# Performance work log

Measured on AMD Instinct MI355X. Metric: run time of the kernel, lower is better.

## Reference

```python
import jax, jax.numpy as jnp
import numpy as np

D = 768          # embed_dim
NH = 12          # num_heads
HD = D // NH     # head_dim = 64
DEPTH = 12
PATCH = 16
IMG = 256
NP_ = (IMG // PATCH) ** 2   # 256 spatial patches
PTOT = NP_ + 1              # 257 tokens per frame (cls + patches)
SCALE = HD ** -0.5
EPS = 1e-5


def _attn(xb, w, b):
    # xb: (B, S, D); w: (D, 3D); b: (3D,)
    B, S, _ = xb.shape
    qkv = (xb @ w + b).reshape(B, S, 3, NH, HD).transpose(2, 0, 3, 1, 4)
    q, k, v = qkv[0], qkv[1], qkv[2]             # each (B, NH, S, HD)
    a = jax.nn.softmax(jnp.einsum('bhqd,bhkd->bhqk', q, k) * SCALE, axis=-1)
    o = jnp.einsum('bhqk,bhkd->bhqd', a, v)      # (B, NH, S, HD)
    return o.transpose(0, 2, 1, 3).reshape(B, S, D)


def setup_inputs() -> dict:
    key = jax.random.key(0)
    ks = jax.random.split(key, 16)
    std = 0.02
    inp = {
        'x': jax.random.normal(ks[0], (2, 16, 3, IMG, IMG), jnp.float32),
        'patch_w': jax.random.normal(ks[1], (D, 3, PATCH, PATCH), jnp.float32) * std,
        'patch_b': jnp.zeros((D,), jnp.float32),
        'cls_token': jax.random.normal(ks[2], (1, 1, D), jnp.float32) * std,
        'pos_embed': jax.random.normal(ks[3], (1, PTOT, D), jnp.float32) * std,
        'time_embed': jax.random.normal(ks[4], (1, 16, D), jnp.float32) * std,
        'wqkv_s': jax.random.normal(ks[5], (DEPTH, D, 3 * D), jnp.float32) * std,
        'bqkv_s': jnp.zeros((DEPTH, 3 * D), jnp.float32),
        'wqkv_t': jax.random.normal(ks[6], (DEPTH, D, 3 * D), jnp.float32) * std,
        'bqkv_t': jnp.zeros((DEPTH, 3 * D), jnp.float32),
        'wproj': jax.random.normal(ks[7], (DEPTH, D, D), jnp.float32) * std,
        'bproj': jnp.zeros((DEPTH, D), jnp.float32),
        'ln_g': jnp.ones((D,), jnp.float32),
        'ln_b': jnp.zeros((D,), jnp.float32),
        'head_w': jax.random.normal(ks[8], (1, D), jnp.float32) * std,
        'head_b': jnp.zeros((1,), jnp.float32),
    }
    return inp


def reference(x, patch_w, patch_b, cls_token, pos_embed, time_embed,
              wqkv_s, bqkv_s, wqkv_t, bqkv_t, wproj, bproj,
              ln_g, ln_b, head_w, head_b):
    N, T, C, H, W = x.shape
    Hp = H // PATCH
    # patch embed: 16x16 stride-16 conv as unfold + matmul
    xp = x.reshape(N * T, C, Hp, PATCH, Hp, PATCH)
    xp = xp.transpose(0, 2, 4, 1, 3, 5).reshape(N * T, NP_, C * PATCH * PATCH)
    tok = xp @ patch_w.reshape(D, -1).T + patch_b          # (N*T, 256, D)
    tok = tok.reshape(N, T, NP_, D)
    cls = jnp.broadcast_to(cls_token, (N, T, 1, D))
    h = jnp.concatenate([cls, tok], axis=2)                # (N, T, 257, D)
    h = h + pos_embed[:, None]                             # (1,1,257,D) broadcast
    h = h + time_embed[:, :T][:, :, None]                  # (1,T,1,D) broadcast
    h = h.reshape(N, T * PTOT, D)

    for i in range(DEPTH):
        x4 = h.reshape(N, T, PTOT, D)
        # spatial attention within each frame
        xs = x4.reshape(N * T, PTOT, D)
        so = _attn(xs, wqkv_s[i], bqkv_s[i]) @ wproj[i] + bproj[i]
        x4 = x4 + so.reshape(N, T, PTOT, D)
        # temporal attention across frames per spatial location
        xt = x4.transpose(0, 2, 1, 3).reshape(N * PTOT, T, D)
        to = _attn(xt, wqkv_t[i], bqkv_t[i]) @ wproj[i] + bproj[i]
        x4 = x4 + to.reshape(N, PTOT, T, D).transpose(0, 2, 1, 3)
        h = x4.reshape(N, T * PTOT, D)

    mu = h.mean(axis=-1, keepdims=True)
    var = ((h - mu) ** 2).mean(axis=-1, keepdims=True)
    h = (h - mu) * jax.lax.rsqrt(var + EPS) * ln_g + ln_b
    cls_tok = h.reshape(N, T, PTOT, D)[:, :, 0, :].mean(axis=1)   # (N, D)
    logits = cls_tok @ head_w.T + head_b                          # (N, 1)
    return logits
```

## Files before the change

kernel.cpp:

```cpp
#include <hip/hip_runtime.h>
#include <hip/hip_bf16.h>
#include <math.h>

namespace {

constexpr int D    = 768;
constexpr int NH   = 12;
constexpr int PTOT = 257;
constexpr int NB   = 2;
constexpr int TT   = 16;
constexpr int NTOK = NB * TT * PTOT;
constexpr int NPAT = NB * TT * 256;
constexpr int QKVD = 3 * D;

typedef short short8  __attribute__((ext_vector_type(8)));
typedef float float4v __attribute__((ext_vector_type(4)));

__device__ __forceinline__ float bf2f(unsigned short u) {
  unsigned v = ((unsigned)u) << 16;
  float f; __builtin_memcpy(&f, &v, 4); return f;
}
__device__ __forceinline__ unsigned short f2bf(float f) {
  unsigned u; __builtin_memcpy(&u, &f, 4);
  u += 0x7FFFu + ((u >> 16) & 1u);
  return (unsigned short)(u >> 16);
}

__device__ __forceinline__ void gload_lds16(const void* g, void* l) {
  __builtin_amdgcn_global_load_lds((const __attribute__((address_space(1))) void*)g,
                                   (__attribute__((address_space(3))) void*)l, 16, 0, 0);
}

__global__ __launch_bounds__(256) void unfold_kernel(const float* __restrict__ x,
                                                     unsigned short* __restrict__ xpb) {
  int idx = blockIdx.x * 256 + threadIdx.x;
  if (idx >= NPAT * D) return;
  int f  = idx % D;
  int pg = idx / D;
  int c = f >> 8;
  int r = f & 255;
  int i = r >> 4, j = r & 15;
  int nt = pg >> 8;
  int s  = pg & 255;
  int hp = s >> 4, wp = s & 15;
  xpb[idx] = f2bf(x[(size_t)(nt * 3 + c) * 65536 + (size_t)(hp * 16 + i) * 256 + (wp * 16 + j)]);
}

__global__ __launch_bounds__(256) void cast_pw(const float* __restrict__ pw,
                                               unsigned short* __restrict__ pwb) {
  int idx = blockIdx.x * 256 + threadIdx.x;
  if (idx >= D * D) return;
  pwb[idx] = f2bf(pw[idx]);
}

__global__ __launch_bounds__(256) void wconv(const float* __restrict__ W,
                                             unsigned short* __restrict__ WT, int N) {
  __shared__ float tile[32][33];
  int l = blockIdx.z;
  const float* w = W + (size_t)l * 768 * N;
  unsigned short* wt = WT + (size_t)l * 768 * N;
  int n0 = blockIdx.x * 32, k0 = blockIdx.y * 32;
  int t = threadIdx.x;
  {
    int r = t >> 3, c4 = (t & 7) * 4;
    float4 v = *(const float4*)(w + (size_t)(k0 + r) * N + n0 + c4);
    tile[r][c4 + 0] = v.x; tile[r][c4 + 1] = v.y;
    tile[r][c4 + 2] = v.z; tile[r][c4 + 3] = v.w;
  }
  __syncthreads();
  {
    int rn = t >> 3, ck = (t & 7) * 4;
    ushort4 o;
    o.x = f2bf(tile[ck + 0][rn]); o.y = f2bf(tile[ck + 1][rn]);
    o.z = f2bf(tile[ck + 2][rn]); o.w = f2bf(tile[ck + 3][rn]);
    *(ushort4*)(wt + (size_t)(n0 + rn) * 768 + k0 + ck) = o;
  }
}

__global__ __launch_bounds__(256) void assemble_kernel(const float* __restrict__ tok,
    const float* __restrict__ cls,
    const float* __restrict__ pos, const float* __restrict__ tim,
    float* __restrict__ h, unsigned short* __restrict__ hb) {
  int idx = blockIdx.x * 256 + threadIdx.x;
  if (idx >= NTOK * D) return;
  int d = idx % D;
  int tokid = idx / D;
  int p  = tokid % PTOT;
  int nt = tokid / PTOT;
  int t  = nt % TT;
  float v = pos[p * D + d] + tim[t * D + d];
  if (p == 0) v += cls[d];
  else        v += tok[(size_t)(nt * 256 + (p - 1)) * D + d];
  h[idx] = v;
  hb[idx] = f2bf(v);
}

__global__ __launch_bounds__(256) void gemm_bf16(
    const unsigned short* __restrict__ A,
    const unsigned short* __restrict__ BT,
    const float* __restrict__ bias,
    unsigned short* __restrict__ Cb,
    float* __restrict__ Hf,
    unsigned short* __restrict__ Hb,
    int M, int N, int mode)
{
  constexpr int K = 768;
  constexpr int NT = K / 32;
  __shared__ unsigned short smem[16384];
  auto As = (unsigned short (*)[128][32])smem;
  auto Bs = (unsigned short (*)[128][32])(smem + 8192);
  auto Ct = (unsigned short (*)[128])smem;
  int tid = threadIdx.x;

  int nwg = gridDim.x * gridDim.y;
  int wg  = blockIdx.y * gridDim.x + blockIdx.x;
  int qq  = nwg >> 3, rr = nwg & 7;
  int xcd = wg & 7, bidx = wg >> 3;
  int newid = (xcd < rr ? xcd * (qq + 1) : rr * (qq + 1) + (xcd - rr) * qq) + bidx;
  int m0 = (newid / gridDim.x) * 128;
  int n0 = (newid % gridDim.x) * 128;

  int w = tid >> 6, lane = tid & 63;
  int quad = lane >> 4, l16 = lane & 15;
  int wm = (w & 1) * 64, wn = (w >> 1) * 64;
  const int lrow = lane >> 2;
  const int scol = (lane & 3) * 8;
  float4v acc[4][4] = {};

  const unsigned short* gA0 = A + (size_t)min(m0 + w * 32 + lrow, M - 1) * K + scol;
  const unsigned short* gA1 = A + (size_t)min(m0 + w * 32 + 16 + lrow, M - 1) * K + scol;
  const unsigned short* gB0 = BT + (size_t)(n0 + w * 32 + lrow) * K + scol;
  const unsigned short* gB1 = BT + (size_t)(n0 + w * 32 + 16 + lrow) * K + scol;

  auto STAGE = [&](int buf, int t) {
    int kk = t * 32;
    gload_lds16(gA0 + kk, &As[buf][w * 32][0]);
    gload_lds16(gA1 + kk, &As[buf][w * 32 + 16][0]);
    gload_lds16(gB0 + kk, &Bs[buf][w * 32][0]);
    gload_lds16(gB1 + kk, &Bs[buf][w * 32 + 16][0]);
  };
  auto COMPUTE = [&](int buf) {
    short8 af[4], bfr[4];
    #pragma unroll
    for (int i = 0; i < 4; ++i) {
      af[i]  = *(const short8*)&As[buf][wm + i * 16 + l16][quad * 8];
      bfr[i] = *(const short8*)&Bs[buf][wn + i * 16 + l16][quad * 8];
    }
    __builtin_amdgcn_s_setprio(1);
    #pragma unroll
    for (int i = 0; i < 4; ++i)
      #pragma unroll
      for (int j = 0; j < 4; ++j)
        acc[i][j] = __builtin_amdgcn_mfma_f32_16x16x32_bf16(af[i], bfr[j], acc[i][j], 0, 0, 0);
    __builtin_amdgcn_s_setprio(0);
  };

  STAGE(0, 0);
  __syncthreads();
  for (int t = 0; t < NT; t += 2) {
    STAGE(1, t + 1);
    COMPUTE(0);
    __syncthreads();
    if (t + 2 < NT) STAGE(0, t + 2);
    COMPUTE(1);
    __syncthreads();
  }

  if (mode == 2) {
    #pragma unroll
    for (int j = 0; j < 4; ++j) {
      int col = n0 + wn + j * 16 + l16;
      float bv = bias[col];
      #pragma unroll
      for (int i = 0; i < 4; ++i) {
        #pragma unroll
        for (int r = 0; r < 4; ++r) {
          int row = m0 + wm + i * 16 + quad * 4 + r;
          if (row < M) Hf[(size_t)row * N + col] = acc[i][j][r] + bv;
        }
      }
    }
    return;
  }

  #pragma unroll
  for (int j = 0; j < 4; ++j) {
    int col = wn + j * 16 + l16;
    float bv = bias[n0 + col];
    int pc = (((col >> 3) ^ quad) << 3) | (col & 7);
    #pragma unroll
    for (int i = 0; i < 4; ++i) {
      #pragma unroll
      for (int r = 0; r < 4; ++r) {
        int row = wm + i * 16 + quad * 4 + r;
        float v = acc[i][j][r] + bv;
        unsigned short ov;
        if (mode == 1) {
          size_t off = (size_t)(m0 + row) * N + (n0 + col);
          if (m0 + row < M) {
            float nv = Hf[off] + v;
            Hf[off] = nv;
            ov = f2bf(nv);
          } else ov = 0;
        } else {
          ov = f2bf(v);
        }
        Ct[row][pc] = ov;
      }
    }
  }
  __syncthreads();
  unsigned short* Ob = (mode == 0) ? Cb : Hb;
  #pragma unroll
  for (int e = 0; e < 8; ++e) {
    int c    = e * 256 + tid;
    int trow = c >> 4, tch = c & 15;
    int grow = m0 + trow;
    if (grow < M) {
      int pch = tch ^ ((trow >> 2) & 3);
      *(uint4*)(Ob + (size_t)grow * N + n0 + tch * 8) = *(const uint4*)&Ct[trow][pch * 8];
    }
  }
}

__global__ __launch_bounds__(256) void attn_spatial3(
    const unsigned short* __restrict__ qkv,
    unsigned short* __restrict__ o)
{
  __shared__ unsigned short Qs[64][72];
  __shared__ unsigned short KVs[64][72];
  __shared__ unsigned short Psl[4][16][72];
  int tid = threadIdx.x;
  int w = tid >> 6, lane = tid & 63;
  int quad = lane >> 4, l16 = lane & 15;
  int bid = blockIdx.x;
  int bh = bid / 5, qt = bid % 5;
  int nt = bh / NH, head = bh % NH;
  int q0 = qt * 64;
  size_t base = (size_t)nt * PTOT;
  const unsigned short* Qg = qkv + head * 64;
  const unsigned short* Kg = qkv + 768 + head * 64;
  const unsigned short* Vg = qkv + 1536 + head * 64;

  #pragma unroll
  for (int e = 0; e < 2; ++e) {
    int chunk = e * 256 + tid;
    int row = chunk >> 3, off = (chunk & 7) * 8;
    int qr = min(q0 + row, PTOT - 1);
    *(uint4*)&Qs[row][off] = *(const uint4*)(Qg + (base + qr) * (size_t)QKVD + off);
  }
  __syncthreads();
  int qrow = w * 16 + l16;
  short8 qa0 = *(const short8*)&Qs[qrow][quad * 8];
  short8 qa1 = *(const short8*)&Qs[qrow][32 + quad * 8];

  float4v st[17];
  #pragma unroll
  for (int kc = 0; kc < 5; ++kc) {
    __syncthreads();
    #pragma unroll
    for (int e = 0; e < 2; ++e) {
      int chunk = e * 256 + tid;
      int row = chunk >> 3, off = (chunk & 7) * 8;
      int kr = min(kc * 64 + row, PTOT - 1);
      *(uint4*)&KVs[row][off] = *(const uint4*)(Kg + (base + kr) * (size_t)QKVD + off);
    }
    __syncthreads();
    #pragma unroll
    for (int tt = 0; tt < 4; ++tt) {
      int t = kc * 4 + tt;
      if (t < 17) {
        short8 kb0 = *(const short8*)&KVs[tt * 16 + l16][quad * 8];
        short8 kb1 = *(const short8*)&KVs[tt * 16 + l16][32 + quad * 8];
        float4v a = {0.f, 0.f, 0.f, 0.f};
        a = __builtin_amdgcn_mfma_f32_16x16x32_bf16(qa0, kb0, a, 0, 0, 0);
        a = __builtin_amdgcn_mfma_f32_16x16x32_bf16(qa1, kb1, a, 0, 0, 0);
        st[t] = a;
      }
    }
  }
  if (l16 >= 1) {
    st[16][0] = -1e30f; st[16][1] = -1e30f; st[16][2] = -1e30f; st[16][3] = -1e30f;
  }
  float mx[4] = {-1e30f, -1e30f, -1e30f, -1e30f};
  #pragma unroll
  for (int t = 0; t < 17; ++t)
    #pragma unroll
    for (int r = 0; r < 4; ++r) mx[r] = fmaxf(mx[r], st[t][r]);
  #pragma unroll
  for (int off = 1; off < 16; off <<= 1)
    #pragma unroll
    for (int r = 0; r < 4; ++r) mx[r] = fmaxf(mx[r], __shfl_xor(mx[r], off));
  float sm[4] = {0.f, 0.f, 0.f, 0.f};
  #pragma unroll
  for (int t = 0; t < 17; ++t)
    #pragma unroll
    for (int r = 0; r < 4; ++r) {
      float e = __expf((st[t][r] - mx[r]) * 0.125f);
      st[t][r] = e;
      sm[r] += e;
    }
  #pragma unroll
  for (int off = 1; off < 16; off <<= 1)
    #pragma unroll
    for (int r = 0; r < 4; ++r) sm[r] += __shfl_xor(sm[r], off);
  float linv[4];
  #pragma unroll
  for (int r = 0; r < 4; ++r) linv[r] = 1.f / sm[r];

  float4v oacc[4] = {};
  #pragma unroll
  for (int vc = 0; vc < 5; ++vc) {
    __syncthreads();
    #pragma unroll
    for (int e = 0; e < 2; ++e) {
      int chunk = e * 256 + tid;
      int row = chunk >> 3;
      int oo  = chunk & 7;
      int off = oo * 8;
      int vr = min(vc * 64 + row, PTOT - 1);
      uint4 u = *(const uint4*)(Vg + (base + vr) * (size_t)QKVD + off);
      #pragma unroll
      for (int s = 0; s < 8; ++s) {
        int idx = (oo + s) & 7;
        unsigned sel01 = (idx & 2) ? u.y : u.x;
        unsigned sel23 = (idx & 2) ? u.w : u.z;
        unsigned dw    = (idx & 4) ? sel23 : sel01;
        unsigned short val = (idx & 1) ? (unsigned short)(dw >> 16) : (unsigned short)dw;
        KVs[off + idx][row] = val;
      }
    }
    #pragma unroll
    for (int tt = 0; tt < 4; ++tt) {
      int t = vc * 4 + tt;
      #pragma unroll
      for (int r = 0; r < 4; ++r) {
        unsigned short pv = 0;
        if (t < 17) pv = f2bf(st[t][r]);
        Psl[w][quad * 4 + r][tt * 16 + l16] = pv;
      }
    }
    __syncthreads();
    int ksmax = (vc == 4) ? 1 : 2;
    #pragma unroll
    for (int ks = 0; ks < 2; ++ks) {
      if (ks < ksmax) {
        short8 pa = *(const short8*)&Psl[w][l16][ks * 32 + quad * 8];
        #pragma unroll
        for (int j = 0; j < 4; ++j) {
          short8 vb = *(const short8*)&KVs[j * 16 + l16][ks * 32 + quad * 8];
          oacc[j] = __builtin_amdgcn_mfma_f32_16x16x32_bf16(pa, vb, oacc[j], 0, 0, 0);
        }
      }
    }
  }
  #pragma unroll
  for (int r = 0; r < 4; ++r) {
    int qg = q0 + w * 16 + quad * 4 + r;
    if (qg < PTOT) {
      #pragma unroll
      for (int j = 0; j < 4; ++j)
        o[(base + qg) * (size_t)D + head * 64 + j * 16 + l16] = f2bf(oacc[j][r] * linv[r]);
    }
  }
}

__global__ __launch_bounds__(256) void attn_temporal2(const unsigned short* __restrict__ qkv,
                                                      unsigned short* __restrict__ o) {
  __shared__ unsigned short Ps[4][16][32];
  __shared__ unsigned short VT[4][64][32];
  int tid = threadIdx.x;
  int w = tid >> 6, lane = tid & 63;
  int quad = lane >> 4, l16 = lane & 15;
  int s = blockIdx.x * 4 + w;
  int p  = s % PTOT;
  int nh = s / PTOT;
  int n = nh / NH, head = nh % NH;

  {
    ushort4 z = {0, 0, 0, 0};
    *(ushort4*)&Ps[w][lane >> 2][16 + (lane & 3) * 4] = z;
    *(uint4*)&VT[w][lane][16] = (uint4){0, 0, 0, 0};
    *(uint4*)&VT[w][lane][24] = (uint4){0, 0, 0, 0};
  }

  const size_t rstride = (size_t)PTOT * QKVD;
  const unsigned short* base0 = qkv + ((size_t)(n * TT) * PTOT + p) * QKVD + head * 64;

  const unsigned short* qrow = base0 + (size_t)l16 * rstride;
  short8 qa0 = *(const short8*)(qrow + quad * 8);
  short8 qa1 = *(const short8*)(qrow + 32 + quad * 8);
  const unsigned short* krow = qrow + 768;
  short8 kb0 = *(const short8*)(krow + quad * 8);
  short8 kb1 = *(const short8*)(krow + 32 + quad * 8);

  float4v sc = {0.f, 0.f, 0.f, 0.f};
  sc = __builtin_amdgcn_mfma_f32_16x16x32_bf16(qa0, kb0, sc, 0, 0, 0);
  sc = __builtin_amdgcn_mfma_f32_16x16x32_bf16(qa1, kb1, sc, 0, 0, 0);

  float e4[4], mx[4], sm[4];
  #pragma unroll
  for (int r = 0; r < 4; ++r) mx[r] = sc[r] * 0.125f;
  #pragma unroll
  for (int off = 1; off < 16; off <<= 1)
    #pragma unroll
    for (int r = 0; r < 4; ++r) mx[r] = fmaxf(mx[r], __shfl_xor(mx[r], off));
  #pragma unroll
  for (int r = 0; r < 4; ++r) { e4[r] = __expf(sc[r] * 0.125f - mx[r]); sm[r] = e4[r]; }
  #pragma unroll
  for (int off = 1; off < 16; off <<= 1)
    #pragma unroll
    for (int r = 0; r < 4; ++r) sm[r] += __shfl_xor(sm[r], off);
  float linv[4];
  #pragma unroll
  for (int r = 0; r < 4; ++r) linv[r] = 1.f / sm[r];

  #pragma unroll
  for (int r = 0; r < 4; ++r) Ps[w][quad * 4 + r][l16] = f2bf(e4[r]);

  {
    const unsigned short* vrow = qrow + 1536 + quad * 16;
    uint4 v0 = *(const uint4*)vrow;
    uint4 v1 = *(const uint4*)(vrow + 8);
    const unsigned short* pv0 = (const unsigned short*)&v0;
    const unsigned short* pv1 = (const unsigned short*)&v1;
    #pragma unroll
    for (int i = 0; i < 8; ++i) VT[w][quad * 16 + i][l16]     = pv0[i];
    #pragma unroll
    for (int i = 0; i < 8; ++i) VT[w][quad * 16 + 8 + i][l16] = pv1[i];
  }

  short8 pa = *(const short8*)&Ps[w][l16][quad * 8];
  float4v oacc[4];
  #pragma unroll
  for (int j = 0; j < 4; ++j) {
    short8 vb = *(const short8*)&VT[w][j * 16 + l16][quad * 8];
    float4v z = {0.f, 0.f, 0.f, 0.f};
    oacc[j] = __builtin_amdgcn_mfma_f32_16x16x32_bf16(pa, vb, z, 0, 0, 0);
  }

  #pragma unroll
  for (int r = 0; r < 4; ++r) {
    size_t orow = ((size_t)(n * TT + quad * 4 + r) * PTOT + p) * D + head * 64;
    #pragma unroll
    for (int j = 0; j < 4; ++j)
      o[orow + j * 16 + l16] = f2bf(oacc[j][r] * linv[r]);
  }
}

__device__ __forceinline__ float block_sum(float v, float* lds) {
  #pragma unroll
  for (int off = 32; off; off >>= 1) v += __shfl_down(v, off);
  __syncthreads();
  if ((threadIdx.x & 63) == 0) lds[threadIdx.x >> 6] = v;
  __syncthreads();
  return lds[0] + lds[1] + lds[2] + lds[3];
}

__global__ __launch_bounds__(256) void head_kernel(const float* __restrict__ h,
    const float* __restrict__ g, const float* __restrict__ b,
    const float* __restrict__ hw, const float* __restrict__ hb,
    float* __restrict__ out) {
  __shared__ float lds[4];
  int n = blockIdx.x, tid = threadIdx.x;
  float logit = 0.f;
  for (int t = 0; t < TT; ++t) {
    const float* row = h + (size_t)((n * TT + t) * PTOT) * D;
    float v[3]; float s = 0.f;
    #pragma unroll
    for (int i = 0; i < 3; ++i) { v[i] = row[tid + 256 * i]; s += v[i]; }
    s = block_sum(s, lds);
    float mu = s * (1.f / D);
    float s2 = 0.f;
    #pragma unroll
    for (int i = 0; i < 3; ++i) { float d0 = v[i] - mu; s2 += d0 * d0; }
    s2 = block_sum(s2, lds);
    float rstd = rsqrtf(s2 * (1.f / D) + 1e-5f);
    float dot = 0.f;
    #pragma unroll
    for (int i = 0; i < 3; ++i) {
      int d0 = tid + 256 * i;
      float y = (v[i] - mu) * rstd * g[d0] + b[d0];
      dot += y * hw[d0];
    }
    dot = block_sum(dot, lds);
    logit += dot;
  }
  if (tid == 0) out[n] = logit * (1.f / TT) + hb[0];
}

}

extern "C" void kernel_launch(void* const* d_in, const int* in_sizes, int n_in,
                              void* d_out, int out_size, void* d_ws, size_t ws_size,
                              hipStream_t stream) {
  const float* x       = (const float*)d_in[0];
  const float* patch_w = (const float*)d_in[1];
  const float* patch_b = (const float*)d_in[2];
  const float* cls     = (const float*)d_in[3];
  const float* pos     = (const float*)d_in[4];
  const float* tim     = (const float*)d_in[5];
  const float* wqkv_s  = (const float*)d_in[6];
  const float* bqkv_s  = (const float*)d_in[7];
  const float* wqkv_t  = (const float*)d_in[8];
  const float* bqkv_t  = (const float*)d_in[9];
  const float* wproj   = (const float*)d_in[10];
  const float* bproj   = (const float*)d_in[11];
  const float* ln_g    = (const float*)d_in[12];
  const float* ln_b    = (const float*)d_in[13];
  const float* head_w  = (const float*)d_in[14];
  const float* head_b  = (const float*)d_in[15];
  float* out = (float*)d_out;

  char* p = (char*)d_ws;
  float* h = (float*)p;                 p += (size_t)NTOK * D * 4;
  unsigned short* hb = (unsigned short*)p;   p += (size_t)NTOK * D * 2;
  unsigned short* qkvb = (unsigned short*)p; p += (size_t)NTOK * QKVD * 2;
  unsigned short* ob = (unsigned short*)p;   p += (size_t)NTOK * D * 2;
  unsigned short* wsT = (unsigned short*)p;  p += (size_t)12 * QKVD * D * 2;
  unsigned short* wtT = (unsigned short*)p;  p += (size_t)12 * QKVD * D * 2;
  unsigned short* wpT = (unsigned short*)p;  p += (size_t)12 * D * D * 2;
  unsigned short* xpb = qkvb;
  unsigned short* pwb = ob;
  float* tok = (float*)wsT;

  unfold_kernel<<<(NPAT * D + 255) / 256, 256, 0, stream>>>(x, xpb);
  cast_pw<<<(D * D + 255) / 256, 256, 0, stream>>>(patch_w, pwb);
  gemm_bf16<<<dim3(D / 128, NPAT / 128), 256, 0, stream>>>(
      xpb, pwb, patch_b, nullptr, tok, nullptr, NPAT, D, 2);
  assemble_kernel<<<(NTOK * D + 255) / 256, 256, 0, stream>>>(tok, cls, pos, tim, h, hb);

  wconv<<<dim3(QKVD / 32, D / 32, 12), 256, 0, stream>>>(wqkv_s, wsT, QKVD);
  wconv<<<dim3(QKVD / 32, D / 32, 12), 256, 0, stream>>>(wqkv_t, wtT, QKVD);
  wconv<<<dim3(D / 32, D / 32, 12), 256, 0, stream>>>(wproj, wpT, D);

  const int MB = (NTOK + 127) / 128;
  for (int l = 0; l < 12; ++l) {
    gemm_bf16<<<dim3(QKVD / 128, MB), 256, 0, stream>>>(
        hb, wsT + (size_t)l * QKVD * D, bqkv_s + (size_t)l * QKVD,
        qkvb, nullptr, nullptr, NTOK, QKVD, 0);
    attn_spatial3<<<NB * TT * NH * 5, 256, 0, stream>>>(qkvb, ob);
    gemm_bf16<<<dim3(D / 128, MB), 256, 0, stream>>>(
        ob, wpT + (size_t)l * D * D, bproj + (size_t)l * D,
        nullptr, h, hb, NTOK, D, 1);

    gemm_bf16<<<dim3(QKVD / 128, MB), 256, 0, stream>>>(
        hb, wtT + (size_t)l * QKVD * D, bqkv_t + (size_t)l * QKVD,
        qkvb, nullptr, nullptr, NTOK, QKVD, 0);
    attn_temporal2<<<(NB * NH * PTOT) / 4, 256, 0, stream>>>(qkvb, ob);
    gemm_bf16<<<dim3(D / 128, MB), 256, 0, stream>>>(
        ob, wpT + (size_t)l * D * D, bproj + (size_t)l * D,
        nullptr, h, hb, NTOK, D, 1);
  }

  head_kernel<<<2, 256, 0, stream>>>(h, ln_g, ln_b, head_w, head_b, out);
}
```

Measured before the change: 2.867 ms.

## Add wide 128x256-tile QKV GEMM with XCD-aware block remapping

```diff
diff --git a/kernel.cpp b/kernel.cpp
--- a/kernel.cpp
+++ b/kernel.cpp
@@ -220,6 +220,113 @@
       int pch = tch ^ ((trow >> 2) & 3);
       *(uint4*)(Ob + (size_t)grow * N + n0 + tch * 8) = *(const uint4*)&Ct[trow][pch * 8];
     }
+  }
+}
+
+__global__ __launch_bounds__(256, 2) void gemm_bf16_wide(
+    const unsigned short* __restrict__ A,
+    const unsigned short* __restrict__ BT,
+    const float* __restrict__ bias,
+    unsigned short* __restrict__ Cb,
+    int M, int N)
+{
+  constexpr int K = 768;
+  constexpr int NT = K / 32;
+  __shared__ unsigned short smem[24576];
+  auto As = (unsigned short (*)[128][32])smem;
+  auto Bs = (unsigned short (*)[256][32])(smem + 8192);
+  auto Ct = (unsigned short (*)[128])smem;
+  int tid = threadIdx.x;
+
+  int nwg = gridDim.x * gridDim.y;
+  int wg  = blockIdx.y * gridDim.x + blockIdx.x;
+  int qq  = nwg >> 3, rr = nwg & 7;
+  int xcd = wg & 7, bidx = wg >> 3;
+  int newid = (xcd < rr ? xcd * (qq + 1) : rr * (qq + 1) + (xcd - rr) * qq) + bidx;
+  int m0 = (newid / gridDim.x) * 128;
+  int n0 = (newid % gridDim.x) * 256;
+
+  int w = tid >> 6, lane = tid & 63;
+  int quad = lane >> 4, l16 = lane & 15;
+  int wm = (w & 1) * 64, wn = (w >> 1) * 128;
+  const int lrow = lane >> 2;
+  const int scol = (lane & 3) * 8;
+  float4v acc[4][8] = {};
+
+  const unsigned short* gA0 = A + (size_t)min(m0 + w * 32 + lrow, M - 1) * K + scol;
+  const unsigned short* gA1 = A + (size_t)min(m0 + w * 32 + 16 + lrow, M - 1) * K + scol;
+  const unsigned short* gB[4];
+  #pragma unroll
+  for (int e = 0; e < 4; ++e)
+    gB[e] = BT + (size_t)(n0 + w * 64 + e * 16 + lrow) * K + scol;
+
+  auto STAGE = [&](int buf, int t) {
+    int kk = t * 32;
+    gload_lds16(gA0 + kk, &As[buf][w * 32][0]);
+    gload_lds16(gA1 + kk, &As[buf][w * 32 + 16][0]);
+    #pragma unroll
+    for (int e = 0; e < 4; ++e)
+      gload_lds16(gB[e] + kk, &Bs[buf][w * 64 + e * 16][0]);
+  };
+  auto COMPUTE = [&](int buf) {
+    short8 af[4], bfr[8];
+    #pragma unroll
+    for (int i = 0; i < 4; ++i)
+      af[i] = *(const short8*)&As[buf][wm + i * 16 + l16][quad * 8];
+    #pragma unroll
+    for (int j = 0; j < 8; ++j)
+      bfr[j] = *(const short8*)&Bs[buf][wn + j * 16 + l16][quad * 8];
+    __builtin_amdgcn_s_setprio(1);
+    #pragma unroll
+    for (int i = 0; i < 4; ++i)
+      #pragma unroll
+      for (int j = 0; j < 8; ++j)
+        acc[i][j] = __builtin_amdgcn_mfma_f32_16x16x32_bf16(af[i], bfr[j], acc[i][j], 0, 0, 0);
+    __builtin_amdgcn_s_setprio(0);
+  };
+
+  STAGE(0, 0);
+  __syncthreads();
+  for (int t = 0; t < NT; t += 2) {
+    STAGE(1, t + 1);
+    COMPUTE(0);
+    __syncthreads();
+    if (t + 2 < NT) STAGE(0, t + 2);
+    COMPUTE(1);
+    __syncthreads();
+  }
+
+  #pragma unroll
+  for (int nh = 0; nh < 2; ++nh) {
+    if ((w >> 1) == nh) {
+      #pragma unroll
+      for (int j = 0; j < 8; ++j) {
+        int col = j * 16 + l16;
+        float bv = bias[n0 + nh * 128 + col];
+        int pc = (((col >> 3) ^ quad) << 3) | (col & 7);
+        #pragma unroll
+        for (int i = 0; i < 4; ++i) {
+          #pragma unroll
+          for (int r = 0; r < 4; ++r) {
+            int row = wm + i * 16 + quad * 4 + r;
+            Ct[row][pc] = f2bf(acc[i][j][r] + bv);
+          }
+        }
+      }
+    }
+    __syncthreads();
+    #pragma unroll
+    for (int e = 0; e < 8; ++e) {
+      int c = e * 256 + tid;
+      int trow = c >> 4, tch = c & 15;
+      int grow = m0 + trow;
+      if (grow < M) {
+        int pch = tch ^ ((trow >> 2) & 3);
+        *(uint4*)(Cb + (size_t)grow * N + n0 + nh * 128 + tch * 8) =
+            *(const uint4*)&Ct[trow][pch * 8];
+      }
+    }
+    __syncthreads();
   }
 }
 
@@ -536,17 +643,17 @@
 
   const int MB = (NTOK + 127) / 128;
   for (int l = 0; l < 12; ++l) {
-    gemm_bf16<<<dim3(QKVD / 128, MB), 256, 0, stream>>>(
+    gemm_bf16_wide<<<dim3(QKVD / 256, MB), 256, 0, stream>>>(
         hb, wsT + (size_t)l * QKVD * D, bqkv_s + (size_t)l * QKVD,
-        qkvb, nullptr, nullptr, NTOK, QKVD, 0);
+        qkvb, NTOK, QKVD);
     attn_spatial3<<<NB * TT * NH * 5, 256, 0, stream>>>(qkvb, ob);
     gemm_bf16<<<dim3(D / 128, MB), 256, 0, stream>>>(
         ob, wpT + (size_t)l * D * D, bproj + (size_t)l * D,
         nullptr, h, hb, NTOK, D, 1);
 
-    gemm_bf16<<<dim3(QKVD / 128, MB), 256, 0, stream>>>(
+    gemm_bf16_wide<<<dim3(QKVD / 256, MB), 256, 0, stream>>>(
         hb, wtT + (size_t)l * QKVD * D, bqkv_t + (size_t)l * QKVD,
-        qkvb, nullptr, nullptr, NTOK, QKVD, 0);
+        qkvb, NTOK, QKVD);
     attn_temporal2<<<(NB * NH * PTOT) / 4, 256, 0, stream>>>(qkvb, ob);
     gemm_bf16<<<dim3(D / 128, MB), 256, 0, stream>>>(
         ob, wpT + (size_t)l * D * D, bproj + (size_t)l * D,
```

Result: slower. 2.983 ms (+4.1%).
